# Optimization experiments

Measured on AMD Instinct MI355X. Metric: run time of the kernel, lower is better.

The kernel has to match this reference:

```python
import jax, jax.numpy as jnp
import numpy as np

B, T, C = 4, 2048, 1024
NH = 16
HD = C // NH
ROPE_BASE = 10000.0


def setup_inputs() -> dict:
    key = jax.random.key(0)
    k1, k2, k3, k4, k5 = jax.random.split(key, 5)
    s = 1.0 / np.sqrt(C)
    return {
        "x": jax.random.normal(k1, (B, T, C), dtype=jnp.float32),
        "W_qkv": jax.random.normal(k2, (C, 3 * C), dtype=jnp.float32) * s,
        "b_qkv": jax.random.normal(k3, (3 * C,), dtype=jnp.float32) * 0.02,
        "W_proj": jax.random.normal(k4, (C, C), dtype=jnp.float32) * s,
        "b_proj": jax.random.normal(k5, (C,), dtype=jnp.float32) * 0.02,
    }


def _rotate_half(u):
    u1, u2 = u[..., : HD // 2], u[..., HD // 2 :]
    return jnp.concatenate((-u2, u1), axis=-1)


def _rope_cos_sin(t, dtype):
    # inv_freq: [HD/2]; positions: [T]
    inv_freq = 1.0 / (ROPE_BASE ** (jnp.arange(0, HD, 2, dtype=jnp.float32) / HD))
    pos = jnp.arange(t, dtype=jnp.float32)
    freqs = pos[:, None] * inv_freq[None, :]          # [T, HD/2]
    emb = jnp.concatenate((freqs, freqs), axis=-1)    # [T, HD]
    return jnp.cos(emb).astype(dtype), jnp.sin(emb).astype(dtype)


def reference(x, W_qkv, b_qkv, W_proj, b_proj):
    b, t, c = x.shape
    qkv = x @ W_qkv + b_qkv                           # [B,T,3C]
    q, k, v = jnp.split(qkv, 3, axis=-1)
    # [B,T,C] -> [B,NH,T,HD]
    def to_heads(u):
        return u.reshape(b, t, NH, HD).transpose(0, 2, 1, 3)
    q, k, v = to_heads(q), to_heads(k), to_heads(v)
    cos, sin = _rope_cos_sin(t, x.dtype)              # [T,HD] each; broadcast over B,NH
    q = q * cos + _rotate_half(q) * sin
    k = k * cos + _rotate_half(k) * sin
    att = jnp.einsum("bhqd,bhkd->bhqk", q, k) * (1.0 / np.sqrt(HD))
    causal = jnp.tril(jnp.ones((t, t), dtype=bool))
    att = jnp.where(causal, att, -jnp.inf)
    att = jax.nn.softmax(att, axis=-1)
    y = jnp.einsum("bhqk,bhkd->bhqd", att, v)         # [B,NH,T,HD]
    y = y.transpose(0, 2, 1, 3).reshape(b, t, c)
    return y @ W_proj + b_proj
```

## Files before the change

kernel.cpp:

```cpp
#include <hip/hip_runtime.h>
#include <cstdint>
#include <cstddef>

typedef __attribute__((ext_vector_type(8))) short short8;
typedef __attribute__((ext_vector_type(4))) float float4x;
typedef __attribute__((ext_vector_type(16))) float float16x;
typedef __attribute__((ext_vector_type(2))) unsigned int uint2v;

__device__ __forceinline__ uint16_t f2b(float f){
  uint32_t u = __builtin_bit_cast(uint32_t, f);
  u += 0x7FFFu + ((u >> 16) & 1u);
  return (uint16_t)(u >> 16);
}
__device__ __forceinline__ float b2f(uint16_t h){
  uint32_t u = ((uint32_t)h) << 16;
  return __builtin_bit_cast(float, u);
}
__device__ __forceinline__ float4x zero4(){
  float4x v; v[0]=0.f; v[1]=0.f; v[2]=0.f; v[3]=0.f; return v;
}
__device__ __forceinline__ float16x zero16(){
  float16x v;
#pragma unroll
  for (int i = 0; i < 16; i++) v[i] = 0.f;
  return v;
}
__device__ __forceinline__ uint32_t cvtpk(float lo, float hi){
  uint32_t r;
  asm("v_cvt_pk_bf16_f32 %0, %1, %2" : "=v"(r) : "v"(lo), "v"(hi));
  return r;
}
__device__ __forceinline__ void plswap(uint32_t &a, uint32_t &b){
#if __has_builtin(__builtin_amdgcn_permlane32_swap)
  uint2v r = __builtin_amdgcn_permlane32_swap(a, b, false, false);
  a = r[0]; b = r[1];
#else
  uint32_t a2 = (uint32_t)__shfl_xor((int)a, 32, 64);
  uint32_t b2 = (uint32_t)__shfl_xor((int)b, 32, 64);
  bool lo = ((threadIdx.x & 63) < 32);
  uint32_t an = lo ? a : b2;
  uint32_t bn = lo ? a2 : b;
  a = an; b = bn;
#endif
}
__device__ __forceinline__ float fexp2(float x){
#if __has_builtin(__builtin_amdgcn_exp2f)
  return __builtin_amdgcn_exp2f(x);
#else
  return exp2f(x);
#endif
}
__device__ __forceinline__ void gload16(const uint16_t* g, uint16_t* l){
  __builtin_amdgcn_global_load_lds(
      (const __attribute__((address_space(1))) uint32_t*)g,
      (__attribute__((address_space(3))) uint32_t*)l, 16, 0, 0);
}

__global__ __launch_bounds__(256) void k_f32_to_bf16(const float* __restrict__ in,
                                                     uint16_t* __restrict__ out, int n4){
  int i = blockIdx.x * 256 + threadIdx.x;
  if (i < n4){
    float4 v = ((const float4*)in)[i];
    ushort4 o;
    o.x = f2b(v.x); o.y = f2b(v.y); o.z = f2b(v.z); o.w = f2b(v.w);
    ((ushort4*)out)[i] = o;
  }
}

__global__ __launch_bounds__(256) void k_transpose_bf16(const float* __restrict__ W,
                                                        uint16_t* __restrict__ Wt, int K, int N){
  __shared__ float tile[32][33];
  int k0 = blockIdx.y * 32, n0 = blockIdx.x * 32;
  int c = threadIdx.x & 31, r0 = threadIdx.x >> 5;
  for (int rr = r0; rr < 32; rr += 8)
    tile[rr][c] = W[(size_t)(k0 + rr) * N + n0 + c];
  __syncthreads();
  for (int rr = r0; rr < 32; rr += 8)
    Wt[(size_t)(n0 + rr) * K + k0 + c] = f2b(tile[c][rr]);
}

__global__ __launch_bounds__(256, 3) void k_gemm_qkv(const uint16_t* __restrict__ A,
                                                     const uint16_t* __restrict__ Bt,
                                                     const float* __restrict__ bias,
                                                     uint16_t* __restrict__ qkv,
                                                     uint16_t* __restrict__ vt){
  const int K = 1024;
  __shared__ __align__(16) uint16_t SM[18432];
  uint16_t* As_ = SM;
  uint16_t* Bs_ = SM + 8192;
  const int tid = threadIdx.x, lane = tid & 63, wave = tid >> 6;
  const int wr = wave >> 1, wc = wave & 1;
  const int m0 = blockIdx.y * 128, n0 = blockIdx.x * 128;
  const int quad = lane >> 4, l15 = lane & 15;
  const int rowA = tid >> 2, chA = tid & 3;

  float4x acc[4][4];
  for (int i = 0; i < 4; i++) for (int j = 0; j < 4; j++) acc[i][j] = zero4();

  const uint16_t* pa0 = &A[(size_t)(m0 + rowA)*K + chA*8];
  const uint16_t* pa1 = &A[(size_t)(m0 + rowA + 64)*K + chA*8];
  const uint16_t* pb0 = &Bt[(size_t)(n0 + rowA)*K + chA*8];
  const uint16_t* pb1 = &Bt[(size_t)(n0 + rowA + 64)*K + chA*8];

  gload16(pa0, &As_[tid*8]);
  gload16(pa1, &As_[64*32 + tid*8]);
  gload16(pb0, &Bs_[tid*8]);
  gload16(pb1, &Bs_[64*32 + tid*8]);

  int buf = 0;
  for (int k0 = 0; k0 < K; k0 += 32){
    __syncthreads();
    if (k0 + 32 < K){
      int nb = buf ^ 1;
      gload16(pa0 + k0 + 32, &As_[nb*4096 + tid*8]);
      gload16(pa1 + k0 + 32, &As_[nb*4096 + 64*32 + tid*8]);
      gload16(pb0 + k0 + 32, &Bs_[nb*4096 + tid*8]);
      gload16(pb1 + k0 + 32, &Bs_[nb*4096 + 64*32 + tid*8]);
    }
    short8 af[4], bfr[4];
#pragma unroll
    for (int mt = 0; mt < 4; mt++)
      af[mt] = *(const short8*)&As_[buf*4096 + (wr*64 + mt*16 + l15)*32 + quad*8];
#pragma unroll
    for (int nt = 0; nt < 4; nt++)
      bfr[nt] = *(const short8*)&Bs_[buf*4096 + (wc*64 + nt*16 + l15)*32 + quad*8];
#pragma unroll
    for (int mt = 0; mt < 4; mt++)
#pragma unroll
      for (int nt = 0; nt < 4; nt++)
        acc[mt][nt] = __builtin_amdgcn_mfma_f32_16x16x32_bf16(af[mt], bfr[nt], acc[mt][nt], 0, 0, 0);
    buf ^= 1;
  }

  if (blockIdx.x < 16){
#pragma unroll
    for (int mt = 0; mt < 4; mt++){
      int grow = m0 + wr*64 + mt*16 + quad*4;
      int tpos = grow & 2047;
#pragma unroll
      for (int nt = 0; nt < 2; nt++){
        int gcol = n0 + wc*64 + nt*16 + l15;
        float bv1 = bias[gcol], bv2 = bias[gcol + 32];
        int i = nt*16 + l15;
        float inv = exp2f(-(float)i * 0.4152410118609203f);
#pragma unroll
        for (int r = 0; r < 4; r++){
          float ang = (float)(tpos + r) * inv;
          float s, c;
          __sincosf(ang, &s, &c);
          float u1 = acc[mt][nt][r]   + bv1;
          float u2 = acc[mt][nt+2][r] + bv2;
          qkv[(size_t)(grow + r)*3072 + gcol]      = f2b(u1*c - u2*s);
          qkv[(size_t)(grow + r)*3072 + gcol + 32] = f2b(u2*c + u1*s);
        }
      }
    }
  } else {
    __syncthreads();
    uint16_t* T = &SM[wave*4608];
#pragma unroll
    for (int mt = 0; mt < 4; mt++)
#pragma unroll
      for (int nt = 0; nt < 4; nt++){
        int gcol = n0 + wc*64 + nt*16 + l15;
        float bv = bias[gcol];
#pragma unroll
        for (int r = 0; r < 4; r++)
          T[(nt*16 + l15)*72 + mt*16 + quad*4 + r] = f2b(acc[mt][nt][r] + bv);
      }
    __syncthreads();
    const int h = (n0 + wc*64 - 2048) >> 6;
    const int tg0 = m0 + wr*64;
    const int bb = tg0 >> 11, tb = tg0 & 2047;
    const int bh64 = (bb*16 + h)*64;
    const int d32 = lane & 31, th = lane >> 5;
#pragma unroll
    for (int dd = 0; dd < 2; dd++)
#pragma unroll
      for (int it = 0; it < 4; it++){
        short8 v = *(const short8*)&T[(d32 + 32*dd)*72 + th*32 + it*8];
        *(short8*)&vt[((size_t)(bh64 + d32 + 32*dd))*2048 + tb + th*32 + it*8] = v;
      }
  }
}

__global__ __launch_bounds__(256, 3) void k_gemm_proj(const uint16_t* __restrict__ A,
                                                      const uint16_t* __restrict__ Bt,
                                                      const float* __restrict__ bias,
                                                      float* __restrict__ Cout,
                                                      int M, int N, int K){
  __shared__ __align__(16) uint16_t As[2][128*32];
  __shared__ __align__(16) uint16_t Bs[2][128*32];
  const int tid = threadIdx.x, lane = tid & 63, wave = tid >> 6;
  const int wr = wave >> 1, wc = wave & 1;
  const int m0 = blockIdx.y * 128, n0 = blockIdx.x * 128;
  const int quad = lane >> 4, l15 = lane & 15;
  const int rowA = tid >> 2, chA = tid & 3;

  float4x acc[4][4];
  for (int i = 0; i < 4; i++) for (int j = 0; j < 4; j++) acc[i][j] = zero4();

  const uint16_t* pa0 = &A[(size_t)(m0 + rowA)*K + chA*8];
  const uint16_t* pa1 = &A[(size_t)(m0 + rowA + 64)*K + chA*8];
  const uint16_t* pb0 = &Bt[(size_t)(n0 + rowA)*K + chA*8];
  const uint16_t* pb1 = &Bt[(size_t)(n0 + rowA + 64)*K + chA*8];

  gload16(pa0, &As[0][tid*8]);
  gload16(pa1, &As[0][64*32 + tid*8]);
  gload16(pb0, &Bs[0][tid*8]);
  gload16(pb1, &Bs[0][64*32 + tid*8]);

  int buf = 0;
  for (int k0 = 0; k0 < K; k0 += 32){
    __syncthreads();
    if (k0 + 32 < K){
      int nb = buf ^ 1;
      gload16(pa0 + k0 + 32, &As[nb][tid*8]);
      gload16(pa1 + k0 + 32, &As[nb][64*32 + tid*8]);
      gload16(pb0 + k0 + 32, &Bs[nb][tid*8]);
      gload16(pb1 + k0 + 32, &Bs[nb][64*32 + tid*8]);
    }
    short8 af[4], bfr[4];
#pragma unroll
    for (int mt = 0; mt < 4; mt++)
      af[mt] = *(const short8*)&As[buf][(wr*64 + mt*16 + l15)*32 + quad*8];
#pragma unroll
    for (int nt = 0; nt < 4; nt++)
      bfr[nt] = *(const short8*)&Bs[buf][(wc*64 + nt*16 + l15)*32 + quad*8];
#pragma unroll
    for (int mt = 0; mt < 4; mt++)
#pragma unroll
      for (int nt = 0; nt < 4; nt++)
        acc[mt][nt] = __builtin_amdgcn_mfma_f32_16x16x32_bf16(af[mt], bfr[nt], acc[mt][nt], 0, 0, 0);
    buf ^= 1;
  }

#pragma unroll
  for (int mt = 0; mt < 4; mt++){
    int grow = m0 + wr*64 + mt*16 + quad*4;
#pragma unroll
    for (int nt = 0; nt < 4; nt++){
      int gcol = n0 + wc*64 + nt*16 + l15;
      float bv = bias[gcol];
#pragma unroll
      for (int r = 0; r < 4; r++)
        Cout[(size_t)(grow + r)*N + gcol] = acc[mt][nt][r] + bv;
    }
  }
}

__global__ __launch_bounds__(512) void k_attn(const uint16_t* __restrict__ qkv,
                                              const uint16_t* __restrict__ vt,
                                              uint16_t* __restrict__ y){
  __shared__ __align__(16) uint16_t Klds[2][64*64];
  __shared__ __align__(16) uint16_t Vlds[2][64*64];

  const int Did = blockIdx.x;
  const int g = Did & 7, ii = Did >> 3;
  const int bh = g*8 + (ii >> 2);
  const int X  = ii & 3;
  const int b = bh >> 4, h = bh & 15;
  const int lane = threadIdx.x & 63, w = threadIdx.x >> 6;
  const int l31 = lane & 31, hi = lane >> 5;

  const uint16_t* Qbase  = qkv + (size_t)b*2048*3072 + h*64;
  const uint16_t* Kbase  = qkv + (size_t)b*2048*3072 + 1024 + h*64;
  const uint16_t* Vtbase = vt  + (size_t)bh*64*2048;

  const float S2 = 0.18033688011112042f;
  const float M2 = 43.28085122666890f;

  const int isV  = w >> 2;
  const int rbase = (w & 3) * 16;
  const int rsub = lane >> 3, csub = lane & 7;

  const int cA = X, cB = 7 - X;
  const int KT_A = 4*cA + 4;
  const int TS = 36;

  int c = cA;
  int qr = c*256 + w*32;

  short8 aq[4];
#pragma unroll
  for (int kc = 0; kc < 4; kc++)
    aq[kc] = *(const short8*)&Qbase[(size_t)(qr + l31)*3072 + kc*16 + hi*8];

  float16x o[2];
  o[0] = zero16(); o[1] = zero16();
  float lr4[4] = {0.f, 0.f, 0.f, 0.f};

  auto epilogue = [&](){
    float l = (lr4[0] + lr4[1]) + (lr4[2] + lr4[3]);
    l += __shfl_xor(l, 32, 64);
    float linv = 1.f / l;
    float lv[16];
#pragma unroll
    for (int r = 0; r < 16; r++)
      lv[r] = __shfl(linv, (r&3) + 8*(r>>2) + 4*hi, 64);
#pragma unroll
    for (int dt = 0; dt < 2; dt++)
#pragma unroll
      for (int r = 0; r < 16; r++){
        int row = (r&3) + 8*(r>>2) + 4*hi;
        y[((size_t)(b*2048 + qr + row))*1024 + h*64 + dt*32 + l31] = f2b(o[dt][r] * lv[r]);
      }
  };

#pragma unroll
  for (int j = 0; j < 2; j++){
    int r  = rbase + j*8 + rsub;
    int cg = csub ^ (r & 7);
    if (isV) gload16(Vtbase + (size_t)r*2048 + cg*8, &Vlds[0][(rbase + j*8)*64 + lane*8]);
    else     gload16(Kbase  + (size_t)r*3072 + cg*8, &Klds[0][(rbase + j*8)*64 + lane*8]);
  }

  int cur = 0;
  for (int t = 0; t < TS; ++t){
    __syncthreads();
    const int kt = (t < KT_A) ? t : t - KT_A;
    if (t + 1 < TS){
      const int ktn = (t + 1 < KT_A) ? t + 1 : t + 1 - KT_A;
      int nb = cur ^ 1;
#pragma unroll
      for (int j = 0; j < 2; j++){
        int r  = rbase + j*8 + rsub;
        int cg = csub ^ (r & 7);
        if (isV) gload16(Vtbase + (size_t)r*2048 + (size_t)ktn*64 + cg*8,
                         &Vlds[nb][(rbase + j*8)*64 + lane*8]);
        else     gload16(Kbase  + (size_t)(ktn*64 + r)*3072 + cg*8,
                         &Klds[nb][(rbase + j*8)*64 + lane*8]);
      }
    }

    if (t == KT_A){
      epilogue();
      c = cB; qr = c*256 + w*32;
#pragma unroll
      for (int kc = 0; kc < 4; kc++)
        aq[kc] = *(const short8*)&Qbase[(size_t)(qr + l31)*3072 + kc*16 + hi*8];
      o[0] = zero16(); o[1] = zero16();
      lr4[0] = lr4[1] = lr4[2] = lr4[3] = 0.f;
    }

    if (kt*64 <= qr + 31){
      float16x p0 = zero16(), p1 = zero16();
      __builtin_amdgcn_s_setprio(1);
#pragma unroll
      for (int kc = 0; kc < 4; kc++){
        const int ch = 2*kc + hi;
        short8 ak0 = *(const short8*)&Klds[cur][(l31)*64      + ((ch ^ (l31 & 7))*8)];
        short8 ak1 = *(const short8*)&Klds[cur][(32 + l31)*64 + ((ch ^ (l31 & 7))*8)];
        p0 = __builtin_amdgcn_mfma_f32_32x32x16_bf16(ak0, aq[kc], p0, 0, 0, 0);
        p1 = __builtin_amdgcn_mfma_f32_32x32x16_bf16(ak1, aq[kc], p1, 0, 0, 0);
      }
      __builtin_amdgcn_s_setprio(0);

      if (kt*64 + 63 > qr){
        const int tq = qr + l31;
#pragma unroll
        for (int r = 0; r < 16; r++){
          int kb = kt*64 + (r&3) + 8*(r>>2) + 4*hi;
          if (kb > tq)      p0[r] = -1e30f;
          if (kb + 32 > tq) p1[r] = -1e30f;
        }
      }

#pragma unroll
      for (int r = 0; r < 16; r++){
        float e0 = fexp2(__builtin_fmaf(p0[r], S2, -M2));
        float e1 = fexp2(__builtin_fmaf(p1[r], S2, -M2));
        lr4[r & 3] += e0 + e1;
        p0[r] = e0; p1[r] = e1;
      }

      __builtin_amdgcn_s_setprio(1);
#pragma unroll
      for (int kc = 0; kc < 4; kc++){
        const int e8 = (kc & 1)*8;
        uint32_t w0, w1, w2, w3;
        if (kc < 2){
          w0 = cvtpk(p0[e8+0], p0[e8+1]); w1 = cvtpk(p0[e8+2], p0[e8+3]);
          w2 = cvtpk(p0[e8+4], p0[e8+5]); w3 = cvtpk(p0[e8+6], p0[e8+7]);
        } else {
          w0 = cvtpk(p1[e8+0], p1[e8+1]); w1 = cvtpk(p1[e8+2], p1[e8+3]);
          w2 = cvtpk(p1[e8+4], p1[e8+5]); w3 = cvtpk(p1[e8+6], p1[e8+7]);
        }
        plswap(w0, w2);
        plswap(w1, w3);
        union { uint32_t u[4]; short8 s; } ap;
        ap.u[0] = w0; ap.u[1] = w1; ap.u[2] = w2; ap.u[3] = w3;

        const int ch = 2*kc + hi;
        short8 bv0 = *(const short8*)&Vlds[cur][(l31)*64      + ((ch ^ (l31 & 7))*8)];
        short8 bv1 = *(const short8*)&Vlds[cur][(32 + l31)*64 + ((ch ^ (l31 & 7))*8)];
        o[0] = __builtin_amdgcn_mfma_f32_32x32x16_bf16(ap.s, bv0, o[0], 0, 0, 0);
        o[1] = __builtin_amdgcn_mfma_f32_32x32x16_bf16(ap.s, bv1, o[1], 0, 0, 0);
      }
      __builtin_amdgcn_s_setprio(0);
    }
    cur ^= 1;
  }

  epilogue();
}

extern "C" void kernel_launch(void* const* d_in, const int* in_sizes, int n_in,
                              void* d_out, int out_size, void* d_ws, size_t ws_size,
                              hipStream_t stream){
  const float* x     = (const float*)d_in[0];
  const float* Wqkv  = (const float*)d_in[1];
  const float* bqkv  = (const float*)d_in[2];
  const float* Wproj = (const float*)d_in[3];
  const float* bproj = (const float*)d_in[4];

  uint16_t* p = (uint16_t*)d_ws;
  uint16_t* xb    = p; p += (size_t)8192*1024;
  uint16_t* wqkvt = p; p += (size_t)3072*1024;
  uint16_t* wprjt = p; p += (size_t)1024*1024;
  uint16_t* qkv   = p; p += (size_t)8192*3072;
  uint16_t* vt    = p; p += (size_t)64*64*2048;
  uint16_t* yb    = p; p += (size_t)8192*1024;

  k_f32_to_bf16<<<8192, 256, 0, stream>>>(x, xb, 2097152);
  k_transpose_bf16<<<dim3(96, 32), 256, 0, stream>>>(Wqkv, wqkvt, 1024, 3072);
  k_transpose_bf16<<<dim3(32, 32), 256, 0, stream>>>(Wproj, wprjt, 1024, 1024);
  k_gemm_qkv<<<dim3(24, 64), 256, 0, stream>>>(xb, wqkvt, bqkv, qkv, vt);
  k_attn<<<256, 512, 0, stream>>>(qkv, vt, yb);
  k_gemm_proj<<<dim3(8, 64), 256, 0, stream>>>(yb, wprjt, bproj, (float*)d_out, 8192, 1024, 1024);
}
```

Measured before the change: 251.9 us.

## Restructure QKV GEMM into 256x256 tiles with a multi-stage swizzled LDS pipeline

The QKV projection GEMM moves from 128x128 tiles with 256 threads to 256x256 tiles with 512 threads. It uses a four-slot LDS ring with an XOR swizzle to avoid bank conflicts, explicit vmcnt waits and barriers, and s_setprio around the MFMA blocks. Block IDs are remapped for better L2 reuse, and the V-transpose epilogue is split into two halves. The goal is more data reuse per byte loaded and better overlap of global loads with MFMA work. The cost is higher register and LDS use, which lowers occupancy, and a more fragile hand-written schedule.

```diff
diff --git a/kernel.cpp b/kernel.cpp
--- a/kernel.cpp
+++ b/kernel.cpp
@@ -79,67 +79,106 @@
     Wt[(size_t)(n0 + rr) * K + k0 + c] = f2b(tile[c][rr]);
 }
 
-__global__ __launch_bounds__(256, 3) void k_gemm_qkv(const uint16_t* __restrict__ A,
-                                                     const uint16_t* __restrict__ Bt,
-                                                     const float* __restrict__ bias,
-                                                     uint16_t* __restrict__ qkv,
-                                                     uint16_t* __restrict__ vt){
-  const int K = 1024;
-  __shared__ __align__(16) uint16_t SM[18432];
-  uint16_t* As_ = SM;
-  uint16_t* Bs_ = SM + 8192;
+__global__ __launch_bounds__(512) void k_gemm_qkv(const uint16_t* __restrict__ A,
+                                                  const uint16_t* __restrict__ Bt,
+                                                  const float* __restrict__ bias,
+                                                  uint16_t* __restrict__ qkv,
+                                                  uint16_t* __restrict__ vt){
+  __shared__ __align__(16) uint16_t SM[65536];
   const int tid = threadIdx.x, lane = tid & 63, wave = tid >> 6;
-  const int wr = wave >> 1, wc = wave & 1;
-  const int m0 = blockIdx.y * 128, n0 = blockIdx.x * 128;
+  const int wm = wave >> 2, wn = wave & 3;
   const int quad = lane >> 4, l15 = lane & 15;
-  const int rowA = tid >> 2, chA = tid & 3;
-
-  float4x acc[4][4];
-  for (int i = 0; i < 4; i++) for (int j = 0; j < 4; j++) acc[i][j] = zero4();
-
-  const uint16_t* pa0 = &A[(size_t)(m0 + rowA)*K + chA*8];
-  const uint16_t* pa1 = &A[(size_t)(m0 + rowA + 64)*K + chA*8];
-  const uint16_t* pb0 = &Bt[(size_t)(n0 + rowA)*K + chA*8];
-  const uint16_t* pb1 = &Bt[(size_t)(n0 + rowA + 64)*K + chA*8];
-
-  gload16(pa0, &As_[tid*8]);
-  gload16(pa1, &As_[64*32 + tid*8]);
-  gload16(pb0, &Bs_[tid*8]);
-  gload16(pb1, &Bs_[64*32 + tid*8]);
-
-  int buf = 0;
-  for (int k0 = 0; k0 < K; k0 += 32){
-    __syncthreads();
-    if (k0 + 32 < K){
-      int nb = buf ^ 1;
-      gload16(pa0 + k0 + 32, &As_[nb*4096 + tid*8]);
-      gload16(pa1 + k0 + 32, &As_[nb*4096 + 64*32 + tid*8]);
-      gload16(pb0 + k0 + 32, &Bs_[nb*4096 + tid*8]);
-      gload16(pb1 + k0 + 32, &Bs_[nb*4096 + 64*32 + tid*8]);
-    }
-    short8 af[4], bfr[4];
-#pragma unroll
-    for (int mt = 0; mt < 4; mt++)
-      af[mt] = *(const short8*)&As_[buf*4096 + (wr*64 + mt*16 + l15)*32 + quad*8];
-#pragma unroll
-    for (int nt = 0; nt < 4; nt++)
-      bfr[nt] = *(const short8*)&Bs_[buf*4096 + (wc*64 + nt*16 + l15)*32 + quad*8];
-#pragma unroll
-    for (int mt = 0; mt < 4; mt++)
-#pragma unroll
-      for (int nt = 0; nt < 4; nt++)
-        acc[mt][nt] = __builtin_amdgcn_mfma_f32_16x16x32_bf16(af[mt], bfr[nt], acc[mt][nt], 0, 0, 0);
-    buf ^= 1;
-  }
-
-  if (blockIdx.x < 16){
-#pragma unroll
-    for (int mt = 0; mt < 4; mt++){
-      int grow = m0 + wr*64 + mt*16 + quad*4;
+
+  const int wg = (blockIdx.x & 7) * 48 + (blockIdx.x >> 3);
+  const int bx = wg >> 5, by = wg & 31;
+  const int m0 = by * 256, n0 = bx * 256;
+
+  const int rsr = tid >> 2;
+  const int cg  = (tid & 3) ^ ((tid >> 3) & 3);
+  const size_t aRow0 = (size_t)(m0 + rsr)       * 1024 + cg * 8;
+  const size_t aRow1 = (size_t)(m0 + rsr + 128) * 1024 + cg * 8;
+  const size_t bRow0 = (size_t)(n0 + rsr)       * 1024 + cg * 8;
+  const size_t bRow1 = (size_t)(n0 + rsr + 128) * 1024 + cg * 8;
+  const int d0 = tid * 8, d1 = 4096 + tid * 8;
+  const int mc8 = (quad ^ ((l15 >> 1) & 3)) * 8;
+
+  float4x acc[8][4];
+#pragma unroll
+  for (int i = 0; i < 8; i++)
+#pragma unroll
+    for (int j = 0; j < 4; j++) acc[i][j] = zero4();
+
+#define STAGE_A(T, ch, slot) \
+  gload16(A  + aRow0 + (size_t)((T)*64 + (ch)*32), &SM[(slot)*8192 + d0]); \
+  gload16(A  + aRow1 + (size_t)((T)*64 + (ch)*32), &SM[(slot)*8192 + d1]);
+#define STAGE_B(T, ch, slot) \
+  gload16(Bt + bRow0 + (size_t)((T)*64 + (ch)*32), &SM[32768 + (slot)*8192 + d0]); \
+  gload16(Bt + bRow1 + (size_t)((T)*64 + (ch)*32), &SM[32768 + (slot)*8192 + d1]);
+#define RD_A(rs, mh, j) (*(const short8*)&SM[(rs) + (wm*128 + (mh)*64 + (j)*16 + l15)*32 + mc8])
+#define RD_B(rs, n)     (*(const short8*)&SM[32768 + (rs) + (wn*64 + (n)*16 + l15)*32 + mc8])
+#define MMROW(mi, a8) \
+  acc[mi][0] = __builtin_amdgcn_mfma_f32_16x16x32_bf16(a8, bf[0], acc[mi][0], 0, 0, 0); \
+  acc[mi][1] = __builtin_amdgcn_mfma_f32_16x16x32_bf16(a8, bf[1], acc[mi][1], 0, 0, 0); \
+  acc[mi][2] = __builtin_amdgcn_mfma_f32_16x16x32_bf16(a8, bf[2], acc[mi][2], 0, 0, 0); \
+  acc[mi][3] = __builtin_amdgcn_mfma_f32_16x16x32_bf16(a8, bf[3], acc[mi][3], 0, 0, 0);
+#define MM(mh) \
+  __builtin_amdgcn_s_setprio(1); \
+  MMROW((mh)*4+0, af[0]) MMROW((mh)*4+1, af[1]) MMROW((mh)*4+2, af[2]) MMROW((mh)*4+3, af[3]) \
+  __builtin_amdgcn_s_setprio(0);
+#define BAR() \
+  __builtin_amdgcn_sched_barrier(0); __builtin_amdgcn_s_barrier(); __builtin_amdgcn_sched_barrier(0);
+#define VM8() asm volatile("s_waitcnt vmcnt(8)" ::: "memory");
+
+  STAGE_A(0, 0, 0); STAGE_B(0, 0, 0);
+  STAGE_A(0, 1, 1); STAGE_B(0, 1, 1);
+  STAGE_A(1, 0, 2); STAGE_B(1, 0, 2);
+  VM8(); BAR();
+
+  for (int t = 0; t < 16; ++t){
+    {
+      const int rs = ((2*t) & 3) * 8192;
+      short8 af[4], bf[4];
+      bf[0] = RD_B(rs,0); bf[1] = RD_B(rs,1); bf[2] = RD_B(rs,2); bf[3] = RD_B(rs,3);
+      af[0] = RD_A(rs,0,0); af[1] = RD_A(rs,0,1); af[2] = RD_A(rs,0,2); af[3] = RD_A(rs,0,3);
+      if (t < 15){ STAGE_A(t+1, 1, (2*t+3)&3); }
+      MM(0);
+      BAR();
+      af[0] = RD_A(rs,1,0); af[1] = RD_A(rs,1,1); af[2] = RD_A(rs,1,2); af[3] = RD_A(rs,1,3);
+      if (t < 15){ STAGE_B(t+1, 1, (2*t+3)&3); }
+      MM(1);
+      VM8(); BAR();
+    }
+    {
+      const int rs = ((2*t+1) & 3) * 8192;
+      short8 af[4], bf[4];
+      bf[0] = RD_B(rs,0); bf[1] = RD_B(rs,1); bf[2] = RD_B(rs,2); bf[3] = RD_B(rs,3);
+      af[0] = RD_A(rs,0,0); af[1] = RD_A(rs,0,1); af[2] = RD_A(rs,0,2); af[3] = RD_A(rs,0,3);
+      if (t < 14){ STAGE_A(t+2, 0, (2*t)&3); }
+      MM(0);
+      BAR();
+      af[0] = RD_A(rs,1,0); af[1] = RD_A(rs,1,1); af[2] = RD_A(rs,1,2); af[3] = RD_A(rs,1,3);
+      if (t < 14){ STAGE_B(t+2, 0, (2*t)&3); }
+      MM(1);
+      VM8(); BAR();
+    }
+  }
+#undef STAGE_A
+#undef STAGE_B
+#undef RD_A
+#undef RD_B
+#undef MMROW
+#undef MM
+#undef BAR
+#undef VM8
+
+  if (bx < 8){
+#pragma unroll
+    for (int mt = 0; mt < 8; mt++){
+      int grow = m0 + wm*128 + mt*16 + quad*4;
       int tpos = grow & 2047;
 #pragma unroll
       for (int nt = 0; nt < 2; nt++){
-        int gcol = n0 + wc*64 + nt*16 + l15;
+        int gcol = n0 + wn*64 + nt*16 + l15;
         float bv1 = bias[gcol], bv2 = bias[gcol + 32];
         int i = nt*16 + l15;
         float inv = exp2f(-(float)i * 0.4152410118609203f);
@@ -156,31 +195,34 @@
       }
     }
   } else {
-    __syncthreads();
+    const int h = ((n0 + wn*64) - 2048) >> 6;
+    const int b = m0 >> 11;
+    const int bh64 = (b*16 + h)*64;
     uint16_t* T = &SM[wave*4608];
-#pragma unroll
-    for (int mt = 0; mt < 4; mt++)
-#pragma unroll
-      for (int nt = 0; nt < 4; nt++){
-        int gcol = n0 + wc*64 + nt*16 + l15;
-        float bv = bias[gcol];
-#pragma unroll
-        for (int r = 0; r < 4; r++)
-          T[(nt*16 + l15)*72 + mt*16 + quad*4 + r] = f2b(acc[mt][nt][r] + bv);
-      }
-    __syncthreads();
-    const int h = (n0 + wc*64 - 2048) >> 6;
-    const int tg0 = m0 + wr*64;
-    const int bb = tg0 >> 11, tb = tg0 & 2047;
-    const int bh64 = (bb*16 + h)*64;
     const int d32 = lane & 31, th = lane >> 5;
 #pragma unroll
-    for (int dd = 0; dd < 2; dd++)
-#pragma unroll
-      for (int it = 0; it < 4; it++){
-        short8 v = *(const short8*)&T[(d32 + 32*dd)*72 + th*32 + it*8];
-        *(short8*)&vt[((size_t)(bh64 + d32 + 32*dd))*2048 + tb + th*32 + it*8] = v;
-      }
+    for (int mh = 0; mh < 2; mh++){
+#pragma unroll
+      for (int mq = 0; mq < 4; mq++){
+#pragma unroll
+        for (int nt = 0; nt < 4; nt++){
+          int gcol = n0 + wn*64 + nt*16 + l15;
+          float bv = bias[gcol];
+#pragma unroll
+          for (int r = 0; r < 4; r++)
+            T[(nt*16 + l15)*72 + mq*16 + quad*4 + r] = f2b(acc[mh*4 + mq][nt][r] + bv);
+        }
+      }
+      int tb0 = (m0 & 2047) + wm*128 + mh*64;
+#pragma unroll
+      for (int dd = 0; dd < 2; dd++)
+#pragma unroll
+        for (int it = 0; it < 4; it++){
+          short8 v = *(const short8*)&T[(d32 + 32*dd)*72 + th*32 + it*8];
+          *(short8*)&vt[((size_t)(bh64 + d32 + 32*dd))*2048 + tb0 + th*32 + it*8] = v;
+        }
+      __syncthreads();
+    }
   }
 }
 
@@ -425,7 +467,7 @@
   k_f32_to_bf16<<<8192, 256, 0, stream>>>(x, xb, 2097152);
   k_transpose_bf16<<<dim3(96, 32), 256, 0, stream>>>(Wqkv, wqkvt, 1024, 3072);
   k_transpose_bf16<<<dim3(32, 32), 256, 0, stream>>>(Wproj, wprjt, 1024, 1024);
-  k_gemm_qkv<<<dim3(24, 64), 256, 0, stream>>>(xb, wqkvt, bqkv, qkv, vt);
+  k_gemm_qkv<<<384, 512, 0, stream>>>(xb, wqkvt, bqkv, qkv, vt);
   k_attn<<<256, 512, 0, stream>>>(qkv, vt, yb);
   k_gemm_proj<<<dim3(8, 64), 256, 0, stream>>>(yb, wprjt, bproj, (float*)d_out, 8192, 1024, 1024);
 }
```

Result: slower. 270.7 us (+7.5%).

## Restructure QKV GEMM with 128x256 tiles, 4-stage async pipeline, swizzled LDS

Applied to the files above, without the earlier changes.

Rewrites the QKV projection GEMM to use 512-thread blocks computing 128x256 tiles, a 4-slot LDS ring with three stages in flight, explicit vmcnt waits and raw barriers. It also adds an XOR swizzle on LDS chunks to cut bank conflicts, MFMA priority hints, and a blockIdx remapping so neighbouring blocks sit on different XCDs or share operands. The aim is to hide global load latency and improve operand reuse. The risks are lower occupancy from 96KB of LDS and fragile hand-counted waitcnt logic.

```diff
diff --git a/kernel.cpp b/kernel.cpp
--- a/kernel.cpp
+++ b/kernel.cpp
@@ -79,67 +79,103 @@
     Wt[(size_t)(n0 + rr) * K + k0 + c] = f2b(tile[c][rr]);
 }
 
-__global__ __launch_bounds__(256, 3) void k_gemm_qkv(const uint16_t* __restrict__ A,
-                                                     const uint16_t* __restrict__ Bt,
-                                                     const float* __restrict__ bias,
-                                                     uint16_t* __restrict__ qkv,
-                                                     uint16_t* __restrict__ vt){
-  const int K = 1024;
-  __shared__ __align__(16) uint16_t SM[18432];
-  uint16_t* As_ = SM;
-  uint16_t* Bs_ = SM + 8192;
+__global__ __launch_bounds__(512) void k_gemm_qkv(const uint16_t* __restrict__ A,
+                                                  const uint16_t* __restrict__ Bt,
+                                                  const float* __restrict__ bias,
+                                                  uint16_t* __restrict__ qkv,
+                                                  uint16_t* __restrict__ vt){
+  __shared__ __align__(16) uint16_t SM[49152];
   const int tid = threadIdx.x, lane = tid & 63, wave = tid >> 6;
-  const int wr = wave >> 1, wc = wave & 1;
-  const int m0 = blockIdx.y * 128, n0 = blockIdx.x * 128;
+  const int wm = wave >> 2, wn = wave & 3;
   const int quad = lane >> 4, l15 = lane & 15;
-  const int rowA = tid >> 2, chA = tid & 3;
+
+  const int wg = (blockIdx.x & 7) * 96 + (blockIdx.x >> 3);
+  const int by = wg / 12, bx = wg % 12;
+  const int m0 = by * 128, n0 = bx * 256;
+
+  const int rsr = tid >> 2;
+  const int cg  = (tid & 3) ^ ((tid >> 3) & 3);
+  const size_t aRow  = (size_t)(m0 + rsr)       * 1024 + cg * 8;
+  const size_t bRow0 = (size_t)(n0 + rsr)       * 1024 + cg * 8;
+  const size_t bRow1 = (size_t)(n0 + rsr + 128) * 1024 + cg * 8;
+  const int dA = tid * 8, dB0 = tid * 8, dB1 = 4096 + tid * 8;
+  const int mc8 = (quad ^ ((l15 >> 1) & 3)) * 8;
 
   float4x acc[4][4];
-  for (int i = 0; i < 4; i++) for (int j = 0; j < 4; j++) acc[i][j] = zero4();
-
-  const uint16_t* pa0 = &A[(size_t)(m0 + rowA)*K + chA*8];
-  const uint16_t* pa1 = &A[(size_t)(m0 + rowA + 64)*K + chA*8];
-  const uint16_t* pb0 = &Bt[(size_t)(n0 + rowA)*K + chA*8];
-  const uint16_t* pb1 = &Bt[(size_t)(n0 + rowA + 64)*K + chA*8];
-
-  gload16(pa0, &As_[tid*8]);
-  gload16(pa1, &As_[64*32 + tid*8]);
-  gload16(pb0, &Bs_[tid*8]);
-  gload16(pb1, &Bs_[64*32 + tid*8]);
-
-  int buf = 0;
-  for (int k0 = 0; k0 < K; k0 += 32){
-    __syncthreads();
-    if (k0 + 32 < K){
-      int nb = buf ^ 1;
-      gload16(pa0 + k0 + 32, &As_[nb*4096 + tid*8]);
-      gload16(pa1 + k0 + 32, &As_[nb*4096 + 64*32 + tid*8]);
-      gload16(pb0 + k0 + 32, &Bs_[nb*4096 + tid*8]);
-      gload16(pb1 + k0 + 32, &Bs_[nb*4096 + 64*32 + tid*8]);
-    }
-    short8 af[4], bfr[4];
-#pragma unroll
-    for (int mt = 0; mt < 4; mt++)
-      af[mt] = *(const short8*)&As_[buf*4096 + (wr*64 + mt*16 + l15)*32 + quad*8];
-#pragma unroll
-    for (int nt = 0; nt < 4; nt++)
-      bfr[nt] = *(const short8*)&Bs_[buf*4096 + (wc*64 + nt*16 + l15)*32 + quad*8];
-#pragma unroll
-    for (int mt = 0; mt < 4; mt++)
-#pragma unroll
-      for (int nt = 0; nt < 4; nt++)
-        acc[mt][nt] = __builtin_amdgcn_mfma_f32_16x16x32_bf16(af[mt], bfr[nt], acc[mt][nt], 0, 0, 0);
-    buf ^= 1;
-  }
-
-  if (blockIdx.x < 16){
+#pragma unroll
+  for (int i = 0; i < 4; i++)
+#pragma unroll
+    for (int j = 0; j < 4; j++) acc[i][j] = zero4();
+
+#define STAGE(H) { \
+  const int sl_ = (H) & 3; \
+  gload16(A  + aRow  + (size_t)(H)*32, &SM[sl_*4096 + dA]); \
+  gload16(Bt + bRow0 + (size_t)(H)*32, &SM[16384 + sl_*8192 + dB0]); \
+  gload16(Bt + bRow1 + (size_t)(H)*32, &SM[16384 + sl_*8192 + dB1]); }
+#define LOADFRAGS(SL) \
+  short8 af[4], bf[4]; \
+  bf[0] = *(const short8*)&SM[16384 + (SL)*8192 + (wn*64 +  0 + l15)*32 + mc8]; \
+  bf[1] = *(const short8*)&SM[16384 + (SL)*8192 + (wn*64 + 16 + l15)*32 + mc8]; \
+  bf[2] = *(const short8*)&SM[16384 + (SL)*8192 + (wn*64 + 32 + l15)*32 + mc8]; \
+  bf[3] = *(const short8*)&SM[16384 + (SL)*8192 + (wn*64 + 48 + l15)*32 + mc8]; \
+  af[0] = *(const short8*)&SM[(SL)*4096 + (wm*64 +  0 + l15)*32 + mc8]; \
+  af[1] = *(const short8*)&SM[(SL)*4096 + (wm*64 + 16 + l15)*32 + mc8]; \
+  af[2] = *(const short8*)&SM[(SL)*4096 + (wm*64 + 32 + l15)*32 + mc8]; \
+  af[3] = *(const short8*)&SM[(SL)*4096 + (wm*64 + 48 + l15)*32 + mc8];
+#define MM() { \
+  __builtin_amdgcn_s_setprio(1); \
+  _Pragma("unroll") \
+  for (int mt_ = 0; mt_ < 4; mt_++){ \
+    acc[mt_][0] = __builtin_amdgcn_mfma_f32_16x16x32_bf16(af[mt_], bf[0], acc[mt_][0], 0, 0, 0); \
+    acc[mt_][1] = __builtin_amdgcn_mfma_f32_16x16x32_bf16(af[mt_], bf[1], acc[mt_][1], 0, 0, 0); \
+    acc[mt_][2] = __builtin_amdgcn_mfma_f32_16x16x32_bf16(af[mt_], bf[2], acc[mt_][2], 0, 0, 0); \
+    acc[mt_][3] = __builtin_amdgcn_mfma_f32_16x16x32_bf16(af[mt_], bf[3], acc[mt_][3], 0, 0, 0); \
+  } \
+  __builtin_amdgcn_s_setprio(0); }
+#define BAR() \
+  __builtin_amdgcn_sched_barrier(0); __builtin_amdgcn_s_barrier(); __builtin_amdgcn_sched_barrier(0);
+
+  STAGE(0) STAGE(1) STAGE(2)
+  asm volatile("s_waitcnt vmcnt(6)" ::: "memory");
+  BAR();
+
+  for (int p = 0; p < 29; ++p){
+    const int sl = p & 3;
+    LOADFRAGS(sl)
+    STAGE(p + 3)
+    MM()
+    asm volatile("s_waitcnt vmcnt(6)" ::: "memory");
+    BAR();
+  }
+  {
+    LOADFRAGS(1)
+    MM()
+    asm volatile("s_waitcnt vmcnt(3)" ::: "memory");
+    BAR();
+  }
+  {
+    LOADFRAGS(2)
+    MM()
+    asm volatile("s_waitcnt vmcnt(0)" ::: "memory");
+    BAR();
+  }
+  {
+    LOADFRAGS(3)
+    MM()
+  }
+#undef STAGE
+#undef LOADFRAGS
+#undef MM
+#undef BAR
+
+  if (bx < 8){
 #pragma unroll
     for (int mt = 0; mt < 4; mt++){
-      int grow = m0 + wr*64 + mt*16 + quad*4;
+      int grow = m0 + wm*64 + mt*16 + quad*4;
       int tpos = grow & 2047;
 #pragma unroll
       for (int nt = 0; nt < 2; nt++){
-        int gcol = n0 + wc*64 + nt*16 + l15;
+        int gcol = n0 + wn*64 + nt*16 + l15;
         float bv1 = bias[gcol], bv2 = bias[gcol + 32];
         int i = nt*16 + l15;
         float inv = exp2f(-(float)i * 0.4152410118609203f);
@@ -156,30 +192,30 @@
       }
     }
   } else {
+    const int h = (bx - 8)*4 + wn;
+    const int bb = m0 >> 11;
+    const int tb0 = (m0 & 2047) + wm*64;
+    const int bh64 = (bb*16 + h)*64;
+    uint16_t* T = &SM[wave*4608];
+    const int d32 = lane & 31, th = lane >> 5;
     __syncthreads();
-    uint16_t* T = &SM[wave*4608];
-#pragma unroll
-    for (int mt = 0; mt < 4; mt++)
-#pragma unroll
-      for (int nt = 0; nt < 4; nt++){
-        int gcol = n0 + wc*64 + nt*16 + l15;
-        float bv = bias[gcol];
+#pragma unroll
+    for (int nt = 0; nt < 4; nt++){
+      int gcol = n0 + wn*64 + nt*16 + l15;
+      float bv = bias[gcol];
+#pragma unroll
+      for (int mt = 0; mt < 4; mt++)
 #pragma unroll
         for (int r = 0; r < 4; r++)
           T[(nt*16 + l15)*72 + mt*16 + quad*4 + r] = f2b(acc[mt][nt][r] + bv);
-      }
+    }
     __syncthreads();
-    const int h = (n0 + wc*64 - 2048) >> 6;
-    const int tg0 = m0 + wr*64;
-    const int bb = tg0 >> 11, tb = tg0 & 2047;
-    const int bh64 = (bb*16 + h)*64;
-    const int d32 = lane & 31, th = lane >> 5;
 #pragma unroll
     for (int dd = 0; dd < 2; dd++)
 #pragma unroll
       for (int it = 0; it < 4; it++){
         short8 v = *(const short8*)&T[(d32 + 32*dd)*72 + th*32 + it*8];
-        *(short8*)&vt[((size_t)(bh64 + d32 + 32*dd))*2048 + tb + th*32 + it*8] = v;
+        *(short8*)&vt[((size_t)(bh64 + d32 + 32*dd))*2048 + tb0 + th*32 + it*8] = v;
       }
   }
 }
@@ -425,7 +461,7 @@
   k_f32_to_bf16<<<8192, 256, 0, stream>>>(x, xb, 2097152);
   k_transpose_bf16<<<dim3(96, 32), 256, 0, stream>>>(Wqkv, wqkvt, 1024, 3072);
   k_transpose_bf16<<<dim3(32, 32), 256, 0, stream>>>(Wproj, wprjt, 1024, 1024);
-  k_gemm_qkv<<<dim3(24, 64), 256, 0, stream>>>(xb, wqkvt, bqkv, qkv, vt);
+  k_gemm_qkv<<<768, 512, 0, stream>>>(xb, wqkvt, bqkv, qkv, vt);
   k_attn<<<256, 512, 0, stream>>>(qkv, vt, yb);
   k_gemm_proj<<<dim3(8, 64), 256, 0, stream>>>(yb, wprjt, bproj, (float*)d_out, 8192, 1024, 1024);
 }
```

Result: slower. 259.2 us (+2.9%).
